# Kernel optimization log

Hardware: AMD Instinct MI355X
Metric: run time of the kernel (lower is better)

## Reference

```python
import jax, jax.numpy as jnp
import numpy as np

B, T1, T2, C, H, NIN = 4, 4096, 2048, 512, 8, 3
D = C // H  # head_dim = 64


def setup_inputs() -> dict:
    key = jax.random.key(0)
    ks = jax.random.split(key, 10)
    s = 0.02  # weight init scale
    return {
        "x": jax.random.normal(ks[0], (B, T1, C), jnp.float32),
        "y0": jax.random.normal(ks[1], (B, T2, C), jnp.float32),
        "y1": jax.random.normal(ks[2], (B, T2, C), jnp.float32),
        "y2": jax.random.normal(ks[3], (B, T2, C), jnp.float32),
        "Wq": jax.random.normal(ks[4], (C, C), jnp.float32) * s,
        "bq": jnp.zeros((C,), jnp.float32),
        "Wk": jax.random.normal(ks[5], (NIN, C, C), jnp.float32) * s,
        "bk": jnp.zeros((NIN, C), jnp.float32),
        "Wv": jax.random.normal(ks[6], (NIN, C, C), jnp.float32) * s,
        "bv": jnp.zeros((NIN, C), jnp.float32),
        "Wo": jax.random.normal(ks[7], (C, C), jnp.float32) * s,
        "bo": jnp.zeros((C,), jnp.float32),
    }


def _heads(t, n_head):
    b, n, c = t.shape
    return t.reshape(b, n, n_head, c // n_head).transpose(0, 2, 1, 3)  # [B,H,N,D]


def reference(x, y0, y1, y2, Wq, bq, Wk, bk, Wv, bv, Wo, bo):
    b, t1, c = x.shape
    q = jax.nn.softmax(_heads(x @ Wq.T + bq, H), axis=-1)  # [B,H,T1,D]
    out = q  # note: original initializes accumulator with q itself
    for i, y in enumerate((y0, y1, y2)):
        k = jax.nn.softmax(_heads(y @ Wk[i].T + bk[i], H), axis=-1)  # [B,H,T2,D]
        v = _heads(y @ Wv[i].T + bv[i], H)                            # [B,H,T2,D]
        k_sum = k.sum(axis=-2, keepdims=True)                         # [B,H,1,D]
        D_inv = 1.0 / ((q * k_sum).sum(axis=-1, keepdims=True) + 1e-8)  # [B,H,T1,1]
        context = jnp.einsum('bhnd,bhnv->bhdv', k, v)                 # [B,H,D,D]
        out = out + jnp.einsum('bhqd,bhdv->bhqv', q, context) * D_inv
    out = out.transpose(0, 2, 1, 3).reshape(b, t1, c)
    return out @ Wo.T + bo
```

## Files before the change

kernel.cpp:

```cpp
#include <hip/hip_runtime.h>
#include <stdint.h>

#define B_ 4
#define T1_ 4096
#define T2_ 2048
#define C_ 512
#define H_ 8
#define D_ 64
#define M1_ (B_*T1_)
#define M2_ (B_*T2_)

using f32x4 = __attribute__((ext_vector_type(4))) float;
using bf16x8 = __attribute__((ext_vector_type(8))) __bf16;
using us8 = __attribute__((ext_vector_type(8))) unsigned short;
using us4 = __attribute__((ext_vector_type(4))) unsigned short;

__device__ __forceinline__ unsigned short f2bf(float f){
  unsigned int u = __builtin_bit_cast(unsigned int, f);
  unsigned int r = (u + 0x7fffu + ((u >> 16) & 1u)) >> 16;
  return (unsigned short)r;
}
__device__ __forceinline__ float bf2f(unsigned short u){
  return __builtin_bit_cast(float, ((unsigned int)u) << 16);
}
__device__ __forceinline__ f32x4 mfma16(us8 a, us8 b, f32x4 c){
  return __builtin_amdgcn_mfma_f32_16x16x32_bf16(
      __builtin_bit_cast(bf16x8, a), __builtin_bit_cast(bf16x8, b), c, 0, 0, 0);
}

typedef const __attribute__((address_space(1))) unsigned int gu32;
typedef __attribute__((address_space(3))) unsigned int lu32;
__device__ __forceinline__ void gl_lds16(const void* g, void* l){
  __builtin_amdgcn_global_load_lds((gu32*)g, (lu32*)l, 16, 0, 0);
}

#define WAIT_VM(N) asm volatile("s_waitcnt vmcnt(" #N ")" ::: "memory")
#define RAW_BAR()  { __builtin_amdgcn_s_barrier(); __builtin_amdgcn_sched_barrier(0); }

__device__ __forceinline__ int swz(int row, int blk){ return blk ^ ((row >> 1) & 3); }

__global__ __launch_bounds__(256) void cvt_bf16_4(const float* __restrict__ p0, const float* __restrict__ p1,
                                                  const float* __restrict__ p2, const float* __restrict__ p3,
                                                  unsigned short* o0, unsigned short* o1,
                                                  unsigned short* o2, unsigned short* o3,
                                                  int n0, int n1, int n2, int n3){
  const float* in; unsigned short* out; int n4;
  switch (blockIdx.y){
    case 0: in = p0; out = o0; n4 = n0; break;
    case 1: in = p1; out = o1; n4 = n1; break;
    case 2: in = p2; out = o2; n4 = n2; break;
    default: in = p3; out = o3; n4 = n3; break;
  }
  int i = blockIdx.x * 256 + threadIdx.x;
  if (i >= n4) return;
  f32x4 v = ((const f32x4*)in)[i];
  us4 o;
  #pragma unroll
  for (int j = 0; j < 4; ++j) o[j] = f2bf(v[j]);
  ((us4*)out)[i] = o;
}

__device__ __forceinline__ void tile_write(unsigned short* tile, const f32x4 (&vals)[4][4],
                                           int wr, int wc, int lr, int lk){
  #pragma unroll
  for (int mt = 0; mt < 4; ++mt)
    #pragma unroll
    for (int nt = 0; nt < 4; ++nt)
      #pragma unroll
      for (int r = 0; r < 4; ++r){
        int row = wr*64 + mt*16 + lk*4 + r;
        int cb  = (wc*128 + nt*32 + lr*2) ^ ((row & 7) << 4);
        *(unsigned short*)((char*)tile + row*256 + cb) = f2bf(vals[mt][nt][r]);
      }
}
__device__ __forceinline__ void tile_write_T(unsigned short* tile, const f32x4 (&vals)[4][4],
                                             int wr, int wc, int lr, int lk){
  #pragma unroll
  for (int mt = 0; mt < 4; ++mt)
    #pragma unroll
    for (int nt = 0; nt < 4; ++nt)
      #pragma unroll
      for (int r = 0; r < 4; ++r){
        int n  = wr*64 + mt*16 + lk*4 + r;
        int ch = wc*64 + nt*16 + lr;
        int cb = (n*2) ^ ((ch & 7) << 4);
        *(unsigned short*)((char*)tile + ch*256 + cb) = f2bf(vals[mt][nt][r]);
      }
}
__device__ __forceinline__ void tile_flush(const unsigned short* tile, unsigned short* g,
                                           size_t row0, int col0, int ldg, int t){
  #pragma unroll
  for (int p = 0; p < 8; ++p){
    int row = p*16 + (t >> 4);
    int cb  = ((t & 15) * 16) ^ ((row & 7) << 4);
    us8 v = *(const us8*)((const char*)tile + row*256 + cb);
    *(us8*)(g + (row0 + row) * (size_t)ldg + col0 + (t & 15) * 8) = v;
  }
}

__global__ __launch_bounds__(256, 3) void proj(const unsigned short* __restrict__ xb,
                                               const unsigned short* __restrict__ yball,
                                               const unsigned short* __restrict__ wqb,
                                               const unsigned short* __restrict__ wkb,
                                               const unsigned short* __restrict__ wvb,
                                               const float* __restrict__ bq,
                                               const float* __restrict__ bk,
                                               const float* __restrict__ bv,
                                               unsigned short* __restrict__ qb,
                                               unsigned short* __restrict__ kbT,
                                               unsigned short* __restrict__ vbT,
                                               float* __restrict__ ksum){
  __shared__ unsigned short smem[3*2*4096];
  const int hw = blockIdx.x;
  const int work = (hw & 7) * 256 + (hw >> 3);
  int seg, ii, m0, n0;
  const unsigned short *A, *W;
  const float* bias;
  if (work < 512){
    seg = 0; ii = 0;
    m0 = (work >> 2) << 7; n0 = (work & 3) << 7;
    A = xb; W = wqb; bias = bq;
  } else {
    int r = work - 512;
    int g = r >> 3, s = r & 7;
    ii = g >> 6; m0 = (g & 63) << 7;
    seg = (s < 4) ? 1 : 2;
    n0 = (s & 3) << 7;
    A = yball + (size_t)ii*M2_*C_;
    W = (seg == 1 ? wkb : wvb) + (size_t)ii*C_*C_;
    bias = (seg == 1 ? bk : bv) + (size_t)ii*C_;
  }
  const int t = threadIdx.x;
  const int w = t >> 6, l = t & 63;
  const int wr = w >> 1, wc = w & 1;
  const int lr = l & 15, lk = l >> 4;
  f32x4 acc[4][4] = {};
  auto STAGE = [&](int bb, int k0){
    int c = t, row = c >> 2;
    gl_lds16(A + (size_t)(m0+row)*C_ + k0 + swz(row, c & 3)*8, &smem[bb*8192 + c*8]);
    gl_lds16(W + (size_t)(n0+row)*C_ + k0 + swz(row, c & 3)*8, &smem[bb*8192 + 4096 + c*8]);
    c = t + 256; row = c >> 2;
    gl_lds16(A + (size_t)(m0+row)*C_ + k0 + swz(row, c & 3)*8, &smem[bb*8192 + c*8]);
    gl_lds16(W + (size_t)(n0+row)*C_ + k0 + swz(row, c & 3)*8, &smem[bb*8192 + 4096 + c*8]);
  };
  auto COMPUTE = [&](int bb){
    const unsigned short* sA = &smem[bb*8192];
    const unsigned short* sB = &smem[bb*8192 + 4096];
    us8 af[4], bfr[4];
    #pragma unroll
    for (int mt = 0; mt < 4; ++mt){
      int R = wr*64 + mt*16 + lr;
      af[mt] = *(const us8*)&sA[R*32 + swz(R, lk)*8];
    }
    #pragma unroll
    for (int nt = 0; nt < 4; ++nt){
      int R = wc*64 + nt*16 + lr;
      bfr[nt] = *(const us8*)&sB[R*32 + swz(R, lk)*8];
    }
    __builtin_amdgcn_s_setprio(1);
    #pragma unroll
    for (int mt = 0; mt < 4; ++mt)
      #pragma unroll
      for (int nt = 0; nt < 4; ++nt)
        acc[mt][nt] = mfma16(af[mt], bfr[nt], acc[mt][nt]);
    __builtin_amdgcn_s_setprio(0);
  };
  STAGE(0, 0);
  int cur = 0;
  for (int tt = 0; tt < 15; ++tt){
    int nxt = (cur == 2) ? 0 : cur + 1;
    STAGE(nxt, (tt + 1) * 32);
    WAIT_VM(4);
    RAW_BAR();
    COMPUTE(cur);
    cur = nxt;
  }
  WAIT_VM(0);
  RAW_BAR();
  COMPUTE(cur);
  {
    float bc[4];
    #pragma unroll
    for (int nt = 0; nt < 4; ++nt) bc[nt] = bias[n0 + wc*64 + nt*16 + lr];
    #pragma unroll
    for (int mt = 0; mt < 4; ++mt)
      #pragma unroll
      for (int nt = 0; nt < 4; ++nt)
        #pragma unroll
        for (int r = 0; r < 4; ++r) acc[mt][nt][r] += bc[nt];
  }
  if (seg <= 1){
    #pragma unroll
    for (int mt = 0; mt < 4; ++mt)
      #pragma unroll
      for (int r = 0; r < 4; ++r){
        float m = fmaxf(fmaxf(acc[mt][0][r], acc[mt][1][r]), fmaxf(acc[mt][2][r], acc[mt][3][r]));
        #pragma unroll
        for (int s = 1; s < 16; s <<= 1) m = fmaxf(m, __shfl_xor(m, s, 64));
        float sum = 0.f;
        #pragma unroll
        for (int nt = 0; nt < 4; ++nt){
          float e = __expf(acc[mt][nt][r] - m);
          acc[mt][nt][r] = e; sum += e;
        }
        #pragma unroll
        for (int s = 1; s < 16; s <<= 1) sum += __shfl_xor(sum, s, 64);
        float inv = 1.0f / sum;
        #pragma unroll
        for (int nt = 0; nt < 4; ++nt) acc[mt][nt][r] *= inv;
      }
  }
  if (seg == 1){
    const int b = m0 >> 11;
    #pragma unroll
    for (int nt = 0; nt < 4; ++nt){
      float cs = 0.f;
      #pragma unroll
      for (int mt = 0; mt < 4; ++mt)
        #pragma unroll
        for (int r = 0; r < 4; ++r) cs += acc[mt][nt][r];
      cs += __shfl_xor(cs, 16, 64);
      cs += __shfl_xor(cs, 32, 64);
      if (lk == 0)
        atomicAdd(&ksum[((size_t)ii*B_ + b)*C_ + n0 + wc*64 + nt*16 + lr], cs);
    }
  }
  __syncthreads();
  if (seg == 0){
    tile_write(smem, acc, wr, wc, lr, lk);
    __syncthreads();
    tile_flush(smem, qb, m0, n0, C_, t);
  } else {
    tile_write_T(smem, acc, wr, wc, lr, lk);
    __syncthreads();
    const int b = m0 >> 11;
    const int n_base = m0 & 2047;
    unsigned short* gT = (seg == 1 ? kbT : vbT);
    tile_flush(smem, gT, ((size_t)ii*B_ + b)*C_ + n0, n_base, T2_, t);
  }
}

__global__ __launch_bounds__(256) void ctx_mfma(const unsigned short* __restrict__ kbT,
                                                const unsigned short* __restrict__ vbT,
                                                float* __restrict__ part){
  const int bh = blockIdx.x, kc = blockIdx.y, i = blockIdx.z;
  const int b = bh >> 3, h = bh & 7;
  const size_t rowbase = ((size_t)i*B_ + b)*C_ + h*64;
  const unsigned short* kT = kbT + rowbase*T2_;
  const unsigned short* vT = vbT + rowbase*T2_;
  const int t = threadIdx.x;
  const int w = t >> 6, l = t & 63;
  const int qr = w >> 1, qc = w & 1;
  const int lr = l & 15, lk = l >> 4;
  const int n00 = kc * 256;
  f32x4 acc[2][2] = {};
  #pragma unroll
  for (int it = 0; it < 8; ++it){
    const int k0 = n00 + it*32 + lk*8;
    us8 a0 = *(const us8*)(kT + (size_t)(qr*32 +      lr)*T2_ + k0);
    us8 a1 = *(const us8*)(kT + (size_t)(qr*32 + 16 + lr)*T2_ + k0);
    us8 b0 = *(const us8*)(vT + (size_t)(qc*32 +      lr)*T2_ + k0);
    us8 b1 = *(const us8*)(vT + (size_t)(qc*32 + 16 + lr)*T2_ + k0);
    acc[0][0] = mfma16(a0, b0, acc[0][0]);
    acc[0][1] = mfma16(a0, b1, acc[0][1]);
    acc[1][0] = mfma16(a1, b0, acc[1][0]);
    acc[1][1] = mfma16(a1, b1, acc[1][1]);
  }
  float* dst = part + (((size_t)i*8 + kc)*32 + bh)*4096;
  #pragma unroll
  for (int fa = 0; fa < 2; ++fa)
    #pragma unroll
    for (int fb = 0; fb < 2; ++fb){
      int d0 = qr*32 + fa*16 + lk*4;
      int e  = qc*32 + fb*16 + lr;
      *(f32x4*)(dst + e*64 + d0) = acc[fa][fb];
    }
}

__global__ __launch_bounds__(256) void ctx_reduce(const float* __restrict__ part,
                                                  unsigned short* __restrict__ ctxTb){
  const int bh = blockIdx.x, i = blockIdx.y, t = threadIdx.x;
  for (int idx = t; idx < 4096; idx += 256){
    float s = 0.f;
    #pragma unroll
    for (int kc = 0; kc < 8; ++kc)
      s += part[(((size_t)i*8 + kc)*32 + bh)*4096 + idx];
    ctxTb[((size_t)i*32 + bh)*4096 + idx] = f2bf(s);
  }
}

__global__ __launch_bounds__(256) void combine(const unsigned short* __restrict__ qb,
                                               const unsigned short* __restrict__ ctxTb,
                                               const float* __restrict__ ksum,
                                               unsigned short* __restrict__ omid){
  __shared__ unsigned short tile[128*128];
  const int hw = blockIdx.x;
  const int work = (hw & 7) * 64 + (hw >> 3);
  const int m0 = (work & 127) << 7, n0 = (work >> 7) << 7;
  const int t = threadIdx.x;
  const int w = t >> 6, l = t & 63;
  const int wr = w >> 1, wc = w & 1;
  const int lr = l & 15, lk = l >> 4;
  const int b = m0 >> 12;
  const int bh = b*8 + (n0 >> 6) + wc;
  #pragma unroll
  for (int p = 0; p < 8; ++p){
    int idx = p*256 + t;
    int row = idx >> 4, ch = idx & 15;
    gl_lds16(qb + (size_t)(m0+row)*C_ + n0 + (ch ^ (row & 7))*8, &tile[idx*8]);
  }
  WAIT_VM(0);
  __syncthreads();
  us8 afr[4][2];
  #pragma unroll
  for (int mt = 0; mt < 4; ++mt)
    #pragma unroll
    for (int kk = 0; kk < 2; ++kk){
      int row = wr*64 + mt*16 + lr;
      int ch = wc*8 + kk*4 + lk;
      afr[mt][kk] = *(const us8*)((const char*)tile + row*256 + ((ch ^ (row & 7)) << 4));
    }
  f32x4 acc[4][4];
  #pragma unroll
  for (int mt = 0; mt < 4; ++mt)
    #pragma unroll
    for (int nt = 0; nt < 4; ++nt)
      #pragma unroll
      for (int r = 0; r < 4; ++r){
        int row = wr*64 + mt*16 + lk*4 + r;
        int cbyte = wc*128 + nt*32 + lr*2;
        int ch = cbyte >> 4;
        unsigned short v = *(const unsigned short*)((const char*)tile + row*256 +
                            ((ch ^ (row & 7)) << 4) + (cbyte & 15));
        acc[mt][nt][r] = bf2f(v);
      }
  us8 bden[2];
  #pragma unroll
  for (int kk = 0; kk < 2; ++kk){
    us8 tmp = {};
    if (lr < 3){
      const float* kp = ksum + ((size_t)lr*B_ + b)*C_ + n0 + wc*64 + kk*32 + lk*8;
      f32x4 c0 = *(const f32x4*)kp;
      f32x4 c1 = *(const f32x4*)(kp + 4);
      #pragma unroll
      for (int j = 0; j < 4; ++j){ tmp[j] = f2bf(c0[j]); tmp[4+j] = f2bf(c1[j]); }
    }
    bden[kk] = tmp;
  }
  f32x4 den[4] = {};
  #pragma unroll
  for (int mt = 0; mt < 4; ++mt)
    #pragma unroll
    for (int kk = 0; kk < 2; ++kk)
      den[mt] = mfma16(afr[mt][kk], bden[kk], den[mt]);
  #pragma unroll 1
  for (int i = 0; i < 3; ++i){
    f32x4 dinv[4];
    #pragma unroll
    for (int mt = 0; mt < 4; ++mt)
      #pragma unroll
      for (int r = 0; r < 4; ++r)
        dinv[mt][r] = 1.0f / (__shfl(den[mt][r], (l & 48) | i, 64) + 1e-8f);
    #pragma unroll
    for (int nt = 0; nt < 4; ++nt){
      us8 bfr[2];
      #pragma unroll
      for (int kk = 0; kk < 2; ++kk)
        bfr[kk] = *(const us8*)(ctxTb + ((size_t)(i*32 + bh))*4096 + (nt*16 + lr)*64 + kk*32 + lk*8);
      f32x4 p[4] = {};
      #pragma unroll
      for (int mt = 0; mt < 4; ++mt)
        #pragma unroll
        for (int kk = 0; kk < 2; ++kk)
          p[mt] = mfma16(afr[mt][kk], bfr[kk], p[mt]);
      #pragma unroll
      for (int mt = 0; mt < 4; ++mt)
        #pragma unroll
        for (int r = 0; r < 4; ++r)
          acc[mt][nt][r] += p[mt][r] * dinv[mt][r];
    }
  }
  __syncthreads();
  tile_write(tile, acc, wr, wc, lr, lk);
  __syncthreads();
  tile_flush(tile, omid, m0, n0, C_, t);
}

__global__ __launch_bounds__(256, 3) void gemm_bt(const unsigned short* __restrict__ A,
                                                  const unsigned short* __restrict__ Bw,
                                                  const float* __restrict__ bias,
                                                  float* __restrict__ out){
  __shared__ unsigned short smem[3*2*4096];
  const int hw = blockIdx.x;
  const int work = (hw & 7) * 64 + (hw >> 3);
  const int m0 = ((work >> 2) & 127) << 7, n0 = (work & 3) << 7;
  const int t = threadIdx.x;
  const int w = t >> 6, l = t & 63;
  const int wr = w >> 1, wc = w & 1;
  const int lr = l & 15, lk = l >> 4;
  f32x4 acc[4][4] = {};
  auto STAGE = [&](int bb, int k0){
    int c = t, row = c >> 2;
    gl_lds16(A  + (size_t)(m0+row)*C_ + k0 + swz(row, c & 3)*8, &smem[bb*8192 + c*8]);
    gl_lds16(Bw + (size_t)(n0+row)*C_ + k0 + swz(row, c & 3)*8, &smem[bb*8192 + 4096 + c*8]);
    c = t + 256; row = c >> 2;
    gl_lds16(A  + (size_t)(m0+row)*C_ + k0 + swz(row, c & 3)*8, &smem[bb*8192 + c*8]);
    gl_lds16(Bw + (size_t)(n0+row)*C_ + k0 + swz(row, c & 3)*8, &smem[bb*8192 + 4096 + c*8]);
  };
  auto COMPUTE = [&](int bb){
    const unsigned short* sA = &smem[bb*8192];
    const unsigned short* sB = &smem[bb*8192 + 4096];
    us8 af[4], bfr[4];
    #pragma unroll
    for (int mt = 0; mt < 4; ++mt){
      int R = wr*64 + mt*16 + lr;
      af[mt] = *(const us8*)&sA[R*32 + swz(R, lk)*8];
    }
    #pragma unroll
    for (int nt = 0; nt < 4; ++nt){
      int R = wc*64 + nt*16 + lr;
      bfr[nt] = *(const us8*)&sB[R*32 + swz(R, lk)*8];
    }
    __builtin_amdgcn_s_setprio(1);
    #pragma unroll
    for (int mt = 0; mt < 4; ++mt)
      #pragma unroll
      for (int nt = 0; nt < 4; ++nt)
        acc[mt][nt] = mfma16(af[mt], bfr[nt], acc[mt][nt]);
    __builtin_amdgcn_s_setprio(0);
  };
  STAGE(0, 0);
  int cur = 0;
  for (int tt = 0; tt < 15; ++tt){
    int nxt = (cur == 2) ? 0 : cur + 1;
    STAGE(nxt, (tt + 1) * 32);
    WAIT_VM(4);
    RAW_BAR();
    COMPUTE(cur);
    cur = nxt;
  }
  WAIT_VM(0);
  RAW_BAR();
  COMPUTE(cur);
  #pragma unroll
  for (int mt = 0; mt < 4; ++mt)
    #pragma unroll
    for (int nt = 0; nt < 4; ++nt)
      #pragma unroll
      for (int r = 0; r < 4; ++r){
        int row = m0 + wr*64 + mt*16 + lk*4 + r;
        int col = n0 + wc*64 + nt*16 + lr;
        out[(size_t)row*C_ + col] = acc[mt][nt][r] + bias[col];
      }
}

extern "C" void kernel_launch(void* const* d_in, const int* in_sizes, int n_in,
                              void* d_out, int out_size, void* d_ws, size_t ws_size,
                              hipStream_t stream){
  const float* x  = (const float*)d_in[0];
  const float* y0 = (const float*)d_in[1];
  const float* y1 = (const float*)d_in[2];
  const float* y2 = (const float*)d_in[3];
  const float* Wq = (const float*)d_in[4];
  const float* bq = (const float*)d_in[5];
  const float* Wk = (const float*)d_in[6];
  const float* bk = (const float*)d_in[7];
  const float* Wv = (const float*)d_in[8];
  const float* bv = (const float*)d_in[9];
  const float* Wo = (const float*)d_in[10];
  const float* bo = (const float*)d_in[11];

  char* ws = (char*)d_ws;
  size_t off = 0;
  auto alloc = [&](size_t bytes)->char*{
    char* p = ws + off; off += (bytes + 1023) & ~((size_t)1023); return p;
  };
  unsigned short* xb    = (unsigned short*)alloc((size_t)M1_*C_*2);
  unsigned short* yball = (unsigned short*)alloc((size_t)3*M2_*C_*2);
  unsigned short* wqb   = (unsigned short*)alloc((size_t)C_*C_*2);
  unsigned short* wkb   = (unsigned short*)alloc((size_t)3*C_*C_*2);
  unsigned short* wvb   = (unsigned short*)alloc((size_t)3*C_*C_*2);
  unsigned short* wob   = (unsigned short*)alloc((size_t)C_*C_*2);
  unsigned short* qb    = (unsigned short*)alloc((size_t)M1_*C_*2);
  unsigned short* kbT   = (unsigned short*)alloc((size_t)3*B_*C_*T2_*2);
  unsigned short* vbT   = (unsigned short*)alloc((size_t)3*B_*C_*T2_*2);
  float*          ksum  = (float*)alloc((size_t)3*B_*C_*4);
  float*          part  = (float*)alloc((size_t)3*8*32*4096*4);
  unsigned short* ctxTb = (unsigned short*)alloc((size_t)3*32*4096*2);
  unsigned short* omid  = (unsigned short*)alloc((size_t)M1_*C_*2);

  (void)hipMemsetAsync(ksum, 0, (size_t)3*B_*C_*4, stream);

  cvt_bf16_4<<<dim3(M1_*C_/4/256, 4), 256, 0, stream>>>(
      x, y0, y1, y2, xb, yball, yball + (size_t)M2_*C_, yball + (size_t)2*M2_*C_,
      M1_*C_/4, M2_*C_/4, M2_*C_/4, M2_*C_/4);
  cvt_bf16_4<<<dim3(3*C_*C_/4/256, 4), 256, 0, stream>>>(
      Wq, Wk, Wv, Wo, wqb, wkb, wvb, wob,
      C_*C_/4, 3*C_*C_/4, 3*C_*C_/4, C_*C_/4);

  proj<<<2048, 256, 0, stream>>>(xb, yball, wqb, wkb, wvb, bq, bk, bv, qb, kbT, vbT, ksum);
  ctx_mfma<<<dim3(32, 8, 3), 256, 0, stream>>>(kbT, vbT, part);
  ctx_reduce<<<dim3(32, 3), 256, 0, stream>>>(part, ctxTb);
  combine<<<512, 256, 0, stream>>>(qb, ctxTb, ksum, omid);
  gemm_bt<<<512, 256, 0, stream>>>(omid, wob, bo, (float*)d_out);
}
```

Before: 141.8 us.

## Fuse fp32-to-bf16 activation conversion into projection GEMM loads

Removes the separate activation conversion kernel. The projection GEMM now loads fp32 activations into registers, converts them to bf16 and writes them swizzled into LDS, while weights keep using direct global-to-LDS loads with a reworked prefetch-distance-two pipeline. The output GEMM is also restructured to prefetch two stages ahead with adjusted vmcnt waits. This avoids writing and re-reading the bf16 activation copies, at the cost of more register use and VALU conversion work inside the GEMM main loop.

```diff
diff --git a/kernel.cpp b/kernel.cpp
--- a/kernel.cpp
+++ b/kernel.cpp
@@ -27,6 +27,12 @@
   return __builtin_amdgcn_mfma_f32_16x16x32_bf16(
       __builtin_bit_cast(bf16x8, a), __builtin_bit_cast(bf16x8, b), c, 0, 0, 0);
 }
+__device__ __forceinline__ us8 cvt8(f32x4 a, f32x4 b){
+  us8 v;
+  #pragma unroll
+  for (int j = 0; j < 4; ++j){ v[j] = f2bf(a[j]); v[4+j] = f2bf(b[j]); }
+  return v;
+}
 
 typedef const __attribute__((address_space(1))) unsigned int gu32;
 typedef __attribute__((address_space(3))) unsigned int lu32;
@@ -35,6 +41,7 @@
 }
 
 #define WAIT_VM(N) asm volatile("s_waitcnt vmcnt(" #N ")" ::: "memory")
+#define WAIT_LGKM() asm volatile("s_waitcnt lgkmcnt(0)" ::: "memory")
 #define RAW_BAR()  { __builtin_amdgcn_s_barrier(); __builtin_amdgcn_sched_barrier(0); }
 
 __device__ __forceinline__ int swz(int row, int blk){ return blk ^ ((row >> 1) & 3); }
@@ -98,8 +105,10 @@
   }
 }
 
-__global__ __launch_bounds__(256, 3) void proj(const unsigned short* __restrict__ xb,
-                                               const unsigned short* __restrict__ yball,
+__global__ __launch_bounds__(256, 3) void proj(const float* __restrict__ xf,
+                                               const float* __restrict__ y0f,
+                                               const float* __restrict__ y1f,
+                                               const float* __restrict__ y2f,
                                                const unsigned short* __restrict__ wqb,
                                                const unsigned short* __restrict__ wkb,
                                                const unsigned short* __restrict__ wvb,
@@ -110,23 +119,24 @@
                                                unsigned short* __restrict__ kbT,
                                                unsigned short* __restrict__ vbT,
                                                float* __restrict__ ksum){
-  __shared__ unsigned short smem[3*2*4096];
+  __shared__ unsigned short smem[20480];
   const int hw = blockIdx.x;
   const int work = (hw & 7) * 256 + (hw >> 3);
   int seg, ii, m0, n0;
-  const unsigned short *A, *W;
+  const float* Af;
+  const unsigned short* W;
   const float* bias;
   if (work < 512){
     seg = 0; ii = 0;
     m0 = (work >> 2) << 7; n0 = (work & 3) << 7;
-    A = xb; W = wqb; bias = bq;
+    Af = xf; W = wqb; bias = bq;
   } else {
     int r = work - 512;
     int g = r >> 3, s = r & 7;
     ii = g >> 6; m0 = (g & 63) << 7;
     seg = (s < 4) ? 1 : 2;
     n0 = (s & 3) << 7;
-    A = yball + (size_t)ii*M2_*C_;
+    Af = (ii == 0) ? y0f : (ii == 1 ? y1f : y2f);
     W = (seg == 1 ? wkb : wvb) + (size_t)ii*C_*C_;
     bias = (seg == 1 ? bk : bv) + (size_t)ii*C_;
   }
@@ -134,50 +144,66 @@
   const int w = t >> 6, l = t & 63;
   const int wr = w >> 1, wc = w & 1;
   const int lr = l & 15, lk = l >> 4;
+  const int row0 = t >> 2,          b0 = t & 3;
+  const int row1 = (t + 256) >> 2,  b1 = t & 3;
   f32x4 acc[4][4] = {};
-  auto STAGE = [&](int bb, int k0){
-    int c = t, row = c >> 2;
-    gl_lds16(A + (size_t)(m0+row)*C_ + k0 + swz(row, c & 3)*8, &smem[bb*8192 + c*8]);
-    gl_lds16(W + (size_t)(n0+row)*C_ + k0 + swz(row, c & 3)*8, &smem[bb*8192 + 4096 + c*8]);
-    c = t + 256; row = c >> 2;
-    gl_lds16(A + (size_t)(m0+row)*C_ + k0 + swz(row, c & 3)*8, &smem[bb*8192 + c*8]);
-    gl_lds16(W + (size_t)(n0+row)*C_ + k0 + swz(row, c & 3)*8, &smem[bb*8192 + 4096 + c*8]);
-  };
-  auto COMPUTE = [&](int bb){
-    const unsigned short* sA = &smem[bb*8192];
-    const unsigned short* sB = &smem[bb*8192 + 4096];
-    us8 af[4], bfr[4];
-    #pragma unroll
-    for (int mt = 0; mt < 4; ++mt){
-      int R = wr*64 + mt*16 + lr;
-      af[mt] = *(const us8*)&sA[R*32 + swz(R, lk)*8];
-    }
-    #pragma unroll
-    for (int nt = 0; nt < 4; ++nt){
-      int R = wc*64 + nt*16 + lr;
-      bfr[nt] = *(const us8*)&sB[R*32 + swz(R, lk)*8];
-    }
-    __builtin_amdgcn_s_setprio(1);
-    #pragma unroll
-    for (int mt = 0; mt < 4; ++mt)
-      #pragma unroll
-      for (int nt = 0; nt < 4; ++nt)
-        acc[mt][nt] = mfma16(af[mt], bfr[nt], acc[mt][nt]);
-    __builtin_amdgcn_s_setprio(0);
-  };
-  STAGE(0, 0);
-  int cur = 0;
-  for (int tt = 0; tt < 15; ++tt){
-    int nxt = (cur == 2) ? 0 : cur + 1;
-    STAGE(nxt, (tt + 1) * 32);
-    WAIT_VM(4);
-    RAW_BAR();
-    COMPUTE(cur);
-    cur = nxt;
-  }
-  WAIT_VM(0);
-  RAW_BAR();
-  COMPUTE(cur);
+  f32x4 ar0[4], ar1[4];
+
+#define LOADA(AR, TT) { \
+    const float* ap0 = Af + (size_t)(m0+row0)*C_ + (TT)*32 + b0*8; \
+    const float* ap1 = Af + (size_t)(m0+row1)*C_ + (TT)*32 + b1*8; \
+    AR[0] = *(const f32x4*)ap0; AR[1] = *(const f32x4*)(ap0 + 4); \
+    AR[2] = *(const f32x4*)ap1; AR[3] = *(const f32x4*)(ap1 + 4); }
+#define DSWA(AR, BUF) { \
+    *(us8*)&smem[(BUF)*4096 + row0*32 + swz(row0,b0)*8] = cvt8(AR[0], AR[1]); \
+    *(us8*)&smem[(BUF)*4096 + row1*32 + swz(row1,b1)*8] = cvt8(AR[2], AR[3]); }
+#define GLW(BUF, TT) { \
+    int c=t, row=c>>2; \
+    gl_lds16(W + (size_t)(n0+row)*C_ + (TT)*32 + swz(row,c&3)*8, &smem[8192+(BUF)*4096 + c*8]); \
+    c=t+256; row=c>>2; \
+    gl_lds16(W + (size_t)(n0+row)*C_ + (TT)*32 + swz(row,c&3)*8, &smem[8192+(BUF)*4096 + c*8]); }
+#define PCOMP(S, WB) { \
+    const unsigned short* sA = &smem[(S)*4096]; \
+    const unsigned short* sW = &smem[8192 + (WB)*4096]; \
+    us8 af[4], bfr[4]; \
+    _Pragma("unroll") \
+    for (int mt = 0; mt < 4; ++mt){ int R = wr*64 + mt*16 + lr; af[mt] = *(const us8*)&sA[R*32 + swz(R, lk)*8]; } \
+    _Pragma("unroll") \
+    for (int nt = 0; nt < 4; ++nt){ int R = wc*64 + nt*16 + lr; bfr[nt] = *(const us8*)&sW[R*32 + swz(R, lk)*8]; } \
+    __builtin_amdgcn_s_setprio(1); \
+    _Pragma("unroll") \
+    for (int mt = 0; mt < 4; ++mt) \
+      _Pragma("unroll") \
+      for (int nt = 0; nt < 4; ++nt) \
+        acc[mt][nt] = mfma16(af[mt], bfr[nt], acc[mt][nt]); \
+    __builtin_amdgcn_s_setprio(0); }
+#define PSTEP(T, AR, S) { \
+    WAIT_VM(6); \
+    DSWA(AR, S); \
+    if ((T) + 2 < 16) { LOADA(AR, (T)+2); GLW(((T)+2)%3, (T)+2); } \
+    WAIT_LGKM(); \
+    RAW_BAR(); \
+    PCOMP(S, (T)%3); }
+#define PSTEPL(T, AR, S) { \
+    WAIT_VM(0); \
+    DSWA(AR, S); \
+    WAIT_LGKM(); \
+    RAW_BAR(); \
+    PCOMP(S, (T)%3); }
+
+  LOADA(ar0, 0); GLW(0, 0);
+  LOADA(ar1, 1); GLW(1, 1);
+  PSTEP(0,  ar0, 0) PSTEP(1,  ar1, 1) PSTEP(2,  ar0, 0) PSTEP(3,  ar1, 1)
+  PSTEP(4,  ar0, 0) PSTEP(5,  ar1, 1) PSTEP(6,  ar0, 0) PSTEP(7,  ar1, 1)
+  PSTEP(8,  ar0, 0) PSTEP(9,  ar1, 1) PSTEP(10, ar0, 0) PSTEP(11, ar1, 1)
+  PSTEP(12, ar0, 0) PSTEP(13, ar1, 1) PSTEP(14, ar0, 0) PSTEPL(15, ar1, 1)
+#undef LOADA
+#undef DSWA
+#undef GLW
+#undef PCOMP
+#undef PSTEP
+#undef PSTEPL
+
   {
     float bc[4];
     #pragma unroll
@@ -399,49 +425,44 @@
   const int wr = w >> 1, wc = w & 1;
   const int lr = l & 15, lk = l >> 4;
   f32x4 acc[4][4] = {};
-  auto STAGE = [&](int bb, int k0){
-    int c = t, row = c >> 2;
-    gl_lds16(A  + (size_t)(m0+row)*C_ + k0 + swz(row, c & 3)*8, &smem[bb*8192 + c*8]);
-    gl_lds16(Bw + (size_t)(n0+row)*C_ + k0 + swz(row, c & 3)*8, &smem[bb*8192 + 4096 + c*8]);
-    c = t + 256; row = c >> 2;
-    gl_lds16(A  + (size_t)(m0+row)*C_ + k0 + swz(row, c & 3)*8, &smem[bb*8192 + c*8]);
-    gl_lds16(Bw + (size_t)(n0+row)*C_ + k0 + swz(row, c & 3)*8, &smem[bb*8192 + 4096 + c*8]);
-  };
-  auto COMPUTE = [&](int bb){
-    const unsigned short* sA = &smem[bb*8192];
-    const unsigned short* sB = &smem[bb*8192 + 4096];
-    us8 af[4], bfr[4];
-    #pragma unroll
-    for (int mt = 0; mt < 4; ++mt){
-      int R = wr*64 + mt*16 + lr;
-      af[mt] = *(const us8*)&sA[R*32 + swz(R, lk)*8];
-    }
-    #pragma unroll
-    for (int nt = 0; nt < 4; ++nt){
-      int R = wc*64 + nt*16 + lr;
-      bfr[nt] = *(const us8*)&sB[R*32 + swz(R, lk)*8];
-    }
-    __builtin_amdgcn_s_setprio(1);
-    #pragma unroll
-    for (int mt = 0; mt < 4; ++mt)
-      #pragma unroll
-      for (int nt = 0; nt < 4; ++nt)
-        acc[mt][nt] = mfma16(af[mt], bfr[nt], acc[mt][nt]);
-    __builtin_amdgcn_s_setprio(0);
-  };
-  STAGE(0, 0);
-  int cur = 0;
-  for (int tt = 0; tt < 15; ++tt){
-    int nxt = (cur == 2) ? 0 : cur + 1;
-    STAGE(nxt, (tt + 1) * 32);
-    WAIT_VM(4);
-    RAW_BAR();
-    COMPUTE(cur);
-    cur = nxt;
-  }
-  WAIT_VM(0);
-  RAW_BAR();
-  COMPUTE(cur);
+
+#define GSTAGE(BB, TT) { \
+    int c = t, row = c >> 2; \
+    gl_lds16(A  + (size_t)(m0+row)*C_ + (TT)*32 + swz(row, c & 3)*8, &smem[(BB)*8192 + c*8]); \
+    gl_lds16(Bw + (size_t)(n0+row)*C_ + (TT)*32 + swz(row, c & 3)*8, &smem[(BB)*8192 + 4096 + c*8]); \
+    c = t + 256; row = c >> 2; \
+    gl_lds16(A  + (size_t)(m0+row)*C_ + (TT)*32 + swz(row, c & 3)*8, &smem[(BB)*8192 + c*8]); \
+    gl_lds16(Bw + (size_t)(n0+row)*C_ + (TT)*32 + swz(row, c & 3)*8, &smem[(BB)*8192 + 4096 + c*8]); }
+#define GCOMP(BB) { \
+    const unsigned short* sA = &smem[(BB)*8192]; \
+    const unsigned short* sB = &smem[(BB)*8192 + 4096]; \
+    us8 af[4], bfr[4]; \
+    _Pragma("unroll") \
+    for (int mt = 0; mt < 4; ++mt){ int R = wr*64 + mt*16 + lr; af[mt] = *(const us8*)&sA[R*32 + swz(R, lk)*8]; } \
+    _Pragma("unroll") \
+    for (int nt = 0; nt < 4; ++nt){ int R = wc*64 + nt*16 + lr; bfr[nt] = *(const us8*)&sB[R*32 + swz(R, lk)*8]; } \
+    __builtin_amdgcn_s_setprio(1); \
+    _Pragma("unroll") \
+    for (int mt = 0; mt < 4; ++mt) \
+      _Pragma("unroll") \
+      for (int nt = 0; nt < 4; ++nt) \
+        acc[mt][nt] = mfma16(af[mt], bfr[nt], acc[mt][nt]); \
+    __builtin_amdgcn_s_setprio(0); }
+#define GSTEP(T, N) { \
+    if ((T) + 2 < 16) GSTAGE(((T)+2)%3, (T)+2); \
+    WAIT_VM(N); \
+    RAW_BAR(); \
+    GCOMP((T)%3); }
+
+  GSTAGE(0, 0); GSTAGE(1, 1);
+  GSTEP(0, 8)  GSTEP(1, 8)  GSTEP(2, 8)  GSTEP(3, 8)
+  GSTEP(4, 8)  GSTEP(5, 8)  GSTEP(6, 8)  GSTEP(7, 8)
+  GSTEP(8, 8)  GSTEP(9, 8)  GSTEP(10, 8) GSTEP(11, 8)
+  GSTEP(12, 8) GSTEP(13, 8) GSTEP(14, 4) GSTEP(15, 0)
+#undef GSTAGE
+#undef GCOMP
+#undef GSTEP
+
   #pragma unroll
   for (int mt = 0; mt < 4; ++mt)
     #pragma unroll
@@ -475,8 +496,6 @@
   auto alloc = [&](size_t bytes)->char*{
     char* p = ws + off; off += (bytes + 1023) & ~((size_t)1023); return p;
   };
-  unsigned short* xb    = (unsigned short*)alloc((size_t)M1_*C_*2);
-  unsigned short* yball = (unsigned short*)alloc((size_t)3*M2_*C_*2);
   unsigned short* wqb   = (unsigned short*)alloc((size_t)C_*C_*2);
   unsigned short* wkb   = (unsigned short*)alloc((size_t)3*C_*C_*2);
   unsigned short* wvb   = (unsigned short*)alloc((size_t)3*C_*C_*2);
@@ -491,14 +510,11 @@
 
   (void)hipMemsetAsync(ksum, 0, (size_t)3*B_*C_*4, stream);
 
-  cvt_bf16_4<<<dim3(M1_*C_/4/256, 4), 256, 0, stream>>>(
-      x, y0, y1, y2, xb, yball, yball + (size_t)M2_*C_, yball + (size_t)2*M2_*C_,
-      M1_*C_/4, M2_*C_/4, M2_*C_/4, M2_*C_/4);
   cvt_bf16_4<<<dim3(3*C_*C_/4/256, 4), 256, 0, stream>>>(
       Wq, Wk, Wv, Wo, wqb, wkb, wvb, wob,
       C_*C_/4, 3*C_*C_/4, 3*C_*C_/4, C_*C_/4);
 
-  proj<<<2048, 256, 0, stream>>>(xb, yball, wqb, wkb, wvb, bq, bk, bv, qb, kbT, vbT, ksum);
+  proj<<<2048, 256, 0, stream>>>(x, y0, y1, y2, wqb, wkb, wvb, bq, bk, bv, qb, kbT, vbT, ksum);
   ctx_mfma<<<dim3(32, 8, 3), 256, 0, stream>>>(kbT, vbT, part);
   ctx_reduce<<<dim3(32, 3), 256, 0, stream>>>(part, ctxTb);
   combine<<<512, 256, 0, stream>>>(qb, ctxTb, ksum, omid);
```

Result: faster. 125.2 us (-11.7%).
